# Kernel optimization log

Measured on AMD Instinct MI355X. Metric: run time of the kernel, lower is better.

The kernel has to match this reference:

```python
import jax, jax.numpy as jnp
import numpy as np

BIT = 128
Y_P = 0.5
RIGHT = BIT / 8.0
LEFT = RIGHT / 2.0
UB = BIT / 2.0
ALPHA = 0.1
PCT_NUM, PCT_DEN = 9, 10  # percent = 9/10
C_COEF = (1.0 / RIGHT) * np.log(Y_P / (99.0 * (1.0 - Y_P)))  # slope c (constant since y_p fixed)
A_COEF = -1.0 / (LEFT * C_COEF) * np.log(99.0 * Y_P / (1.0 - Y_P))  # hard-branch factor a
# with y_p=0.5: d = -c*BP, g = -a*c*BP, so f_easy = c*(x-BP), f_hard = a*c*(x-BP)


def setup_inputs() -> dict:
    key = jax.random.key(0)
    k1, k2 = jax.random.split(key)
    N, C = 6144, 200
    u = jax.random.normal(k1, (N, BIT), dtype=jnp.float32)
    labels = jax.random.randint(k2, (N,), 0, C)
    y = jax.nn.one_hot(labels, C, dtype=jnp.int32)
    ind = jnp.arange(N, dtype=jnp.int32)  # unused dataset indices
    return {"u": u, "y": y, "ind": ind}


def reference(u, y, ind):
    sg = jax.lax.stop_gradient
    N = u.shape[0]
    uh = jnp.tanh(u)
    s = (y @ y.T) > 0                      # [N,N] bool similarity (diagonal is True)
    inner = uh @ uh.T                      # [N,N]
    n_sim = s.sum(axis=1)                  # int per-row similar count
    n_dis = N - n_sim
    fn_sim = n_sim.astype(jnp.float32)
    fn_dis = n_dis.astype(jnp.float32)
    idx = jnp.arange(N)[None, :]

    meanS = jnp.clip(jnp.where(s, inner, 0.0).sum(1) / jnp.maximum(fn_sim, 1.0), 0.0, UB)
    meanDS = jnp.clip(jnp.where(s, 0.0, inner).sum(1) / jnp.maximum(fn_dis, 1.0), 0.0, UB)

    dis_sorted = jnp.sort(jnp.where(s, -jnp.inf, inner), axis=1)
    start_dis = (n_dis * PCT_NUM) // PCT_DEN          # int(len*0.9)
    tail_mask = idx >= (N - n_dis + start_dis)[:, None]
    tail_cnt = jnp.maximum((n_dis - start_dis).astype(jnp.float32), 1.0)
    dMax = jnp.clip(jnp.where(tail_mask, dis_sorted, 0.0).sum(1) / tail_cnt, 0.0, UB)

    sim_sorted = jnp.sort(jnp.where(s, inner, jnp.inf), axis=1)
    start_sim = (n_sim * PCT_NUM) // PCT_DEN
    head_mask = idx < (n_sim - start_sim)[:, None]
    head_cnt = jnp.maximum((n_sim - start_sim).astype(jnp.float32), 1.0)
    sMin = jnp.clip(jnp.where(head_mask, sim_sorted, 0.0).sum(1) / head_cnt, 0.0, UB)

    # .item() in the original detaches these -> stop_gradient
    meanS, meanDS, dMax, sMin = map(sg, (meanS, meanDS, dMax, sMin))
    BP = meanS - (UB - meanS) / UB * jnp.abs(meanS - dMax)      # [N]
    BPd = meanDS + meanDS / UB * jnp.abs(meanDS - sMin)         # [N]

    # similar-pair loss: f + log(1+exp(-f)) == softplus(f)
    dc = inner - BP[:, None]
    f_sim = jnp.where(inner > BP[:, None], C_COEF * dc, A_COEF * C_COEF * dc)
    mask_sim = s & (inner != BP[:, None])             # == BP excluded in torch indexing
    cnt_sim = jnp.maximum(mask_sim.sum(1).astype(jnp.float32), 1.0)
    row_pos = jnp.where(mask_sim, jax.nn.softplus(f_sim), 0.0).sum(1) / cnt_sim

    # dissimilar-pair loss: log(1+exp(-f)) == softplus(-f)
    dcd = inner - BPd[:, None]
    f_dis = jnp.where(inner < BPd[:, None], C_COEF * dcd, A_COEF * C_COEF * dcd)
    mask_dis = (~s) & (inner != BPd[:, None])
    cnt_dis = jnp.maximum(mask_dis.sum(1).astype(jnp.float32), 1.0)
    row_neg = jnp.where(mask_dis, jax.nn.softplus(-f_dis), 0.0).sum(1) / cnt_dis

    valid = (n_sim > 0) & (n_dis > 0)
    count = valid.sum().astype(jnp.float32)
    posL = jnp.where(count > 0, jnp.where(valid, row_pos, 0.0).sum() / jnp.maximum(count, 1.0), 0.0)
    navL = jnp.where(count > 0, jnp.where(valid, row_neg, 0.0).sum() / jnp.maximum(count, 1.0), 0.0)

    q_loss = ALPHA * jnp.mean((uh - jnp.sign(uh)) ** 2)
    return posL + navL + q_loss
```

## Files before the change

### kernel.cpp

```cpp
#include <hip/hip_runtime.h>
#include <cstdint>

#define NROW 6144
#define KDIM 128
#define NLAB 200
#define C_COEF (-0.28719499063341177f)
#define UBV 64.0f

typedef _Float16 f16x8 __attribute__((ext_vector_type(8)));
typedef _Float16 f16x2 __attribute__((ext_vector_type(2)));
typedef float f32x4 __attribute__((ext_vector_type(4)));
typedef __attribute__((address_space(1))) const void as1c_void;
typedef __attribute__((address_space(3))) void as3_void;

union U8 { f16x8 h; unsigned u[4]; f16x2 p[4]; };
union CV16 { _Float16 h; unsigned short us; };

__device__ __forceinline__ float softplus_f(float x){
  return fmaxf(x, 0.f) + __logf(1.f + __expf(-fabsf(x)));
}
__device__ __forceinline__ float waveRedF(float v){
#pragma unroll
  for (int o = 32; o; o >>= 1) v += __shfl_down(v, o, 64);
  return v;
}
__device__ __forceinline__ float bfRedF(float v){
#pragma unroll
  for (int o = 32; o; o >>= 1) v += __shfl_xor(v, o, 64);
  return v;
}
__device__ __forceinline__ int bfRedI(int v){
#pragma unroll
  for (int o = 32; o; o >>= 1) v += __shfl_xor(v, o, 64);
  return v;
}
__device__ __forceinline__ int bfMaxI(int v){
#pragma unroll
  for (int o = 32; o; o >>= 1){ int x = __shfl_xor(v, o, 64); v = v > x ? v : x; }
  return v;
}
__device__ __forceinline__ float bfMaxF(float v){
#pragma unroll
  for (int o = 32; o; o >>= 1) v = fmaxf(v, __shfl_xor(v, o, 64));
  return v;
}
__device__ __forceinline__ float val_of_key(unsigned key){
  unsigned bits = (key & 0x8000u) ? (key ^ 0x8000u) : (key ^ 0xFFFFu);
  CV16 cv; cv.us = (unsigned short)bits;
  return (float)cv.h;
}

__global__ __launch_bounds__(256) void k_labtanh(const int* __restrict__ y,
    unsigned char* __restrict__ lab, int* __restrict__ cnt, int* __restrict__ simIdx,
    const float* __restrict__ u, _Float16* __restrict__ uhswz, float* __restrict__ accf){
  const int bid = blockIdx.x;
  const int tid = threadIdx.x;
  const int NLB = NROW / 4;
  if (bid < NLB){
    const int lane = tid & 63;
    const int row = bid * 4 + (tid >> 6);
    if (lane < NLAB / 4){
      const int4 v = ((const int4*)(y + (size_t)row * NLAB))[lane];
      int t = -1;
      if (v.x != 0) t = 4 * lane;
      if (v.y != 0) t = 4 * lane + 1;
      if (v.z != 0) t = 4 * lane + 2;
      if (v.w != 0) t = 4 * lane + 3;
      if (t >= 0){
        lab[row] = (unsigned char)t;
        int p = atomicAdd(&cnt[t], 1);
        if (p < 512) simIdx[t * 512 + p] = row;
      }
    }
    return;
  }
  const int gid = (bid - NLB) * 256 + tid;
  const int row = gid >> 4;
  const int h = gid & 15;
  const int g = h ^ (row & 7);
  const float* sp = u + (size_t)row * KDIM + g * 8;
  float q = 0.f;
  f16x8 o;
#pragma unroll
  for (int t = 0; t < 8; t++){
    float x = sp[t];
    float e2 = __expf(2.f * x);
    float th = 1.f - 2.f * __builtin_amdgcn_rcpf(e2 + 1.f);
    float sg = (th > 0.f) ? 1.f : ((th < 0.f) ? -1.f : 0.f);
    float d = th - sg;
    q += d * d;
    o[t] = (_Float16)th;
  }
  *(f16x8*)(uhswz + (size_t)row * KDIM + h * 8) = o;
  q = waveRedF(q);
  __shared__ float qb[4];
  if ((tid & 63) == 0) qb[tid >> 6] = q;
  __syncthreads();
  if (tid == 0) atomicAdd(&accf[0], qb[0] + qb[1] + qb[2] + qb[3]);
}

__global__ __launch_bounds__(256) void k_mm(const _Float16* __restrict__ A,
    _Float16* __restrict__ out, int row0, int sym){
  const int bj = blockIdx.x, bi = blockIdx.y;
  if (sym && bi > bj) return;
  __shared__ __align__(16) _Float16 SH[2 * 128 * KDIM];
  _Float16* As = SH;
  _Float16* Bs = SH + 128 * KDIM;
  const int tid = threadIdx.x;
  const int wav = tid >> 6, lane = tid & 63;

  const char* Ag = (const char*)(A + (size_t)(row0 + bi * 128) * KDIM);
  const char* Bg = (const char*)(A + (size_t)(bj * 128) * KDIM);
  char* Asb = (char*)As;
  char* Bsb = (char*)Bs;
#pragma unroll
  for (int t = 0; t < 8; t++){
    const int ub = wav * 8192 + t * 1024;
    __builtin_amdgcn_global_load_lds((as1c_void*)(Ag + ub + lane * 16),
                                     (as3_void*)(Asb + ub), 16, 0, 0);
    __builtin_amdgcn_global_load_lds((as1c_void*)(Bg + ub + lane * 16),
                                     (as3_void*)(Bsb + ub), 16, 0, 0);
  }
  __syncthreads();

  const int quad = lane >> 4, l16 = lane & 15;
  const int wm = (wav >> 1) * 64, wn = (wav & 1) * 64;
  f32x4 acc[4][4];
#pragma unroll
  for (int im = 0; im < 4; im++)
#pragma unroll
    for (int in = 0; in < 4; in++)
      acc[im][in] = (f32x4){0.f, 0.f, 0.f, 0.f};

#pragma unroll
  for (int kb = 0; kb < 4; kb++){
    f16x8 af[4], bf[4];
#pragma unroll
    for (int i = 0; i < 4; i++){
      const int m = wm + i * 16 + l16;
      const int gidx = kb * 4 + quad;
      af[i] = *(const f16x8*)(Asb + m * 256 + ((gidx ^ (m & 7)) << 4));
      const int n = wn + i * 16 + l16;
      bf[i] = *(const f16x8*)(Bsb + n * 256 + ((gidx ^ (n & 7)) << 4));
    }
#pragma unroll
    for (int im = 0; im < 4; im++)
#pragma unroll
      for (int in = 0; in < 4; in++)
        acc[im][in] = __builtin_amdgcn_mfma_f32_16x16x32_f16(af[im], bf[in], acc[im][in], 0, 0, 0);
  }
  __syncthreads();

  _Float16* Cs = SH;
#pragma unroll
  for (int im = 0; im < 4; im++)
#pragma unroll
    for (int in = 0; in < 4; in++)
#pragma unroll
      for (int r = 0; r < 4; r++){
        const int rl = wm + im * 16 + quad * 4 + r;
        const int cl = wn + in * 16 + l16;
        Cs[rl * 132 + cl] = (_Float16)acc[im][in][r];
      }
  __syncthreads();

  _Float16* obase = out + (size_t)(bi * 128) * NROW + (size_t)bj * 128;
  const int s = tid & 15;
#pragma unroll
  for (int i = 0; i < 8; i++){
    const int r = (tid >> 4) + i * 16;
    f16x8 vv = *(const f16x8*)(Cs + r * 132 + s * 8);
    *(f16x8*)(obase + (size_t)r * NROW + s * 8) = vv;
  }

  if (sym && bi != bj){
    __syncthreads();
#pragma unroll
    for (int im = 0; im < 4; im++)
#pragma unroll
      for (int in = 0; in < 4; in++)
#pragma unroll
        for (int r = 0; r < 4; r++){
          const int rl = wm + im * 16 + quad * 4 + r;
          const int cl = wn + in * 16 + l16;
          Cs[cl * 132 + rl] = (_Float16)acc[im][in][r];
        }
    __syncthreads();
    _Float16* obase2 = out + (size_t)(bj * 128) * NROW + (size_t)bi * 128;
#pragma unroll
    for (int i = 0; i < 8; i++){
      const int r = (tid >> 4) + i * 16;
      f16x8 vv = *(const f16x8*)(Cs + r * 132 + s * 8);
      *(f16x8*)(obase2 + (size_t)r * NROW + s * 8) = vv;
    }
  }
}

__global__ __launch_bounds__(256) void k_stats(const _Float16* __restrict__ buf,
    const unsigned char* __restrict__ lab, const int* __restrict__ cnt,
    const int* __restrict__ simIdx, float* __restrict__ rowRes, int row0){
  __shared__ int   histS[4][1028];
  __shared__ float simvS[4][512];
  const int tid = threadIdx.x;
  const int lane = tid & 63;
  const int wav = tid >> 6;
  const int lrow = blockIdx.x * 4 + wav;
  const int row = row0 + lrow;
  const int myl = lab[row];
  const int n_sim = cnt[myl];
  const int n_dis = NROW - n_sim;
  if (n_dis == 0 || n_sim == 0) return;
  const int k1 = n_dis - (n_dis * 9) / 10;
  const int k2 = n_sim - (n_sim * 9) / 10;
  const int ns = (n_sim < 512) ? n_sim : 512;

  int*   hist = histS[wav];
  int*   myh  = hist + (lane >> 4) * 257;
  float* simv = simvS[wav];
#pragma unroll
  for (int r = 0; r < 4; r++) *(int4*)&hist[(lane + 64 * r) * 4] = make_int4(0, 0, 0, 0);
  if (lane == 0) *(int4*)&hist[1024] = make_int4(0, 0, 0, 0);

  const f16x8* src = (const f16x8*)(buf + (size_t)lrow * NROW);
  const _Float16* srcs = buf + (size_t)lrow * NROW;

  float sumAll = 0.f;
  const f16x2 ones = (f16x2){(_Float16)1.f, (_Float16)1.f};
#pragma unroll 2
  for (int it = 0; it < 12; ++it){
    U8 x; x.h = src[it * 64 + lane];
#pragma unroll
    for (int k = 0; k < 4; k++){
      unsigned wv = x.u[k];
      unsigned m = (wv >> 15) & 0x00010001u;
      unsigned key2 = wv ^ 0x80008000u ^ (m * 0x7FFFu);
      atomicAdd(&myh[(key2 >> 8) & 0xFFu], 1);
      atomicAdd(&myh[key2 >> 24], 1);
#if __has_builtin(__builtin_amdgcn_fdot2)
      sumAll = __builtin_amdgcn_fdot2(x.p[k], ones, sumAll, false);
#else
      sumAll += (float)x.h[2 * k] + (float)x.h[2 * k + 1];
#endif
    }
  }

  float sumS = 0.f;
  for (int t = lane; t < ns; t += 64){
    int idx = simIdx[myl * 512 + t];
    CV16 cv; cv.h = srcs[idx];
    unsigned bits = (unsigned)cv.us;
    unsigned key = bits ^ 0x8000u ^ ((bits >> 15) * 0x7FFFu);
    float v = (float)cv.h;
    simv[t] = v; sumS += v;
    atomicAdd(&myh[key >> 8], -1);
  }
  sumAll = bfRedF(sumAll);
  sumS = bfRedF(sumS);
  const float sumD = sumAll - sumS;

  int cArr[4];
#pragma unroll
  for (int d = 0; d < 4; d++){
    const int b = 4 * lane + d;
    cArr[d] = hist[b] + hist[257 + b] + hist[514 + b] + hist[771 + b];
  }
  int part = cArr[0] + cArr[1] + cArr[2] + cArr[3];
  int suf = part;
#pragma unroll
  for (int o = 1; o < 64; o <<= 1){
    int x = __shfl_down(suf, o, 64);
    if (lane + o < 64) suf += x;
  }
  int cum = suf - part;
  int encB = -1, krF = 0;
#pragma unroll
  for (int d = 3; d >= 0; --d){
    int cd = cArr[d];
    if (k1 > cum && k1 <= cum + cd){ encB = 4 * lane + d; krF = k1 - cum; }
    cum += cd;
  }
  const int hbStar = bfMaxI(encB);
  const int kr1 = bfMaxI(krF);

#pragma unroll
  for (int r = 0; r < 4; r++) *(int4*)&hist[(lane + 64 * r) * 4] = make_int4(0, 0, 0, 0);
  if (lane == 0) *(int4*)&hist[1024] = make_int4(0, 0, 0, 0);

  float sAb = 0.f;
#pragma unroll 2
  for (int it = 0; it < 12; ++it){
    U8 x; x.h = src[it * 64 + lane];
#pragma unroll
    for (int k = 0; k < 4; k++){
      unsigned wv = x.u[k];
      unsigned m = (wv >> 15) & 0x00010001u;
      unsigned key2 = wv ^ 0x80008000u ^ (m * 0x7FFFu);
      int hbLo = (key2 >> 8) & 0xFF;
      int hbHi = key2 >> 24;
      if (hbLo > hbStar) sAb += (float)x.h[2 * k];
      else if (hbLo == hbStar) atomicAdd(&myh[key2 & 0xFFu], 1);
      if (hbHi > hbStar) sAb += (float)x.h[2 * k + 1];
      else if (hbHi == hbStar) atomicAdd(&myh[(key2 >> 16) & 0xFFu], 1);
    }
  }
  for (int t = lane; t < ns; t += 64){
    float v = simv[t];
    CV16 cv; cv.h = (_Float16)v;
    unsigned bits = (unsigned)cv.us;
    unsigned key = bits ^ 0x8000u ^ ((bits >> 15) * 0x7FFFu);
    int hb = (int)(key >> 8);
    if (hb > hbStar) sAb -= v;
    else if (hb == hbStar) atomicAdd(&myh[key & 0xFFu], -1);
  }
  sAb = bfRedF(sAb);

  int c2[4];
#pragma unroll
  for (int d = 0; d < 4; d++){
    const int b = 4 * lane + d;
    c2[d] = hist[b] + hist[257 + b] + hist[514 + b] + hist[771 + b];
  }
  part = c2[0] + c2[1] + c2[2] + c2[3];
  suf = part;
#pragma unroll
  for (int o = 1; o < 64; o <<= 1){
    int x = __shfl_down(suf, o, 64);
    if (lane + o < 64) suf += x;
  }
  cum = suf - part;
  int encL = -1, g2F = 0;
#pragma unroll
  for (int d = 3; d >= 0; --d){
    int cd = c2[d];
    if (kr1 > cum && kr1 <= cum + cd){ encL = 4 * lane + d; g2F = cum; }
    cum += cd;
  }
  const int lbStar = bfMaxI(encL);
  const int gt2 = bfMaxI(g2F);
  float sumIn = 0.f;
#pragma unroll
  for (int d = 0; d < 4; d++){
    int lb = 4 * lane + d;
    if (lb > lbStar) sumIn += (float)c2[d] * val_of_key((unsigned)((hbStar << 8) | lb));
  }
  sumIn = bfRedF(sumIn);
  const float piv = val_of_key((unsigned)((hbStar << 8) | lbStar));
  const float dSum = sAb + sumIn + (float)(kr1 - gt2) * piv;

  float fpiv2 = -3e38f; int flt = 0;
  for (int t = lane; t < ns; t += 64){
    float vt = simv[t];
    int lt = 0, eq = 0;
    for (int j = 0; j < ns; j++){
      float vj = simv[j];
      lt += (vj < vt); eq += (vj == vt);
    }
    if (lt < k2 && k2 <= lt + eq){ fpiv2 = vt; flt = lt; }
  }
  const float piv2 = bfMaxF(fpiv2);
  const int ltS = bfMaxI(flt);
  float slt = 0.f;
  for (int t = lane; t < ns; t += 64){
    float v = simv[t];
    if (v < piv2) slt += v;
  }
  slt = bfRedF(slt);
  const float sSum = slt + (float)(k2 - ltS) * piv2;

  const float meanS  = fminf(fmaxf(sumS / fmaxf((float)n_sim, 1.f), 0.f), UBV);
  const float meanDS = fminf(fmaxf(sumD / fmaxf((float)n_dis, 1.f), 0.f), UBV);
  const float dMax   = fminf(fmaxf(dSum / fmaxf((float)k1, 1.f), 0.f), UBV);
  const float sMin   = fminf(fmaxf(sSum / fmaxf((float)k2, 1.f), 0.f), UBV);
  const float BP  = meanS - (UBV - meanS) / UBV * fabsf(meanS - dMax);
  const float BPd = meanDS + meanDS / UBV * fabsf(meanDS - sMin);

  float an = 0.f; int ties = 0;
#pragma unroll 2
  for (int it = 0; it < 12; ++it){
    f16x8 h8 = src[it * 64 + lane];
#pragma unroll
    for (int e = 0; e < 8; e++){
      float v = (float)h8[e];
      float dcd = v - BPd;
      float f = ((dcd < 0.f) ? C_COEF : 2.f * C_COEF) * dcd;
      an += softplus_f(-f);
      ties += (dcd == 0.f);
    }
  }
  float spSim = 0.f; int tiesSim = 0;
  float ap = 0.f, cp = 0.f;
  for (int t = lane; t < ns; t += 64){
    float v = simv[t];
    float dcd = v - BPd;
    if (dcd == 0.f) tiesSim++;
    else {
      float f = ((dcd < 0.f) ? C_COEF : 2.f * C_COEF) * dcd;
      spSim += softplus_f(-f);
    }
    if (v != BP){
      float dc = v - BP;
      float f = (v > BP) ? C_COEF * dc : (2.f * C_COEF) * dc;
      ap += softplus_f(f); cp += 1.f;
    }
  }
  an = bfRedF(an); spSim = bfRedF(spSim);
  const int tiesT = bfRedI(ties);
  const int tiesSimT = bfRedI(tiesSim);
  ap = bfRedF(ap); cp = bfRedF(cp);
  if (lane == 0){
    const float L = __logf(1.f + __expf(-0.f));
    float anF = an - (float)tiesT * L - spSim;
    float cnF = (float)(n_dis - (tiesT - tiesSimT));
    float4 r;
    r.x = ap / fmaxf(cp, 1.f);
    r.y = anF / fmaxf(cnF, 1.f);
    r.z = 1.f;
    r.w = 0.f;
    *(float4*)(rowRes + 4 * (size_t)row) = r;
  }
}

__global__ __launch_bounds__(256) void k_final(const float* __restrict__ accf,
    const float* __restrict__ rowRes, float* __restrict__ out){
  const int tid = threadIdx.x;
  float p = 0.f, n = 0.f, c = 0.f;
  for (int i = tid; i < NROW; i += 256){
    float4 r = *(const float4*)(rowRes + 4 * (size_t)i);
    p += r.x; n += r.y; c += r.z;
  }
  p = bfRedF(p); n = bfRedF(n); c = bfRedF(c);
  __shared__ float sb[12];
  const int wav = tid >> 6;
  if ((tid & 63) == 0){ sb[wav] = p; sb[4 + wav] = n; sb[8 + wav] = c; }
  __syncthreads();
  if (tid == 0){
    p = sb[0] + sb[1] + sb[2] + sb[3];
    n = sb[4] + sb[5] + sb[6] + sb[7];
    c = sb[8] + sb[9] + sb[10] + sb[11];
    float posL = 0.f, navL = 0.f;
    if (c > 0.f){ posL = p / c; navL = n / c; }
    out[0] = posL + navL + 0.1f * (accf[0] / (float)(NROW * KDIM));
  }
}

extern "C" void kernel_launch(void* const* d_in, const int* in_sizes, int n_in,
                              void* d_out, int out_size, void* d_ws, size_t ws_size,
                              hipStream_t stream){
  const float* u = (const float*)d_in[0];
  const int* y = (const int*)d_in[1];
  char* ws = (char*)d_ws;
  float* accf = (float*)ws;
  int* cnt = (int*)(ws + 64);
  float* rowRes = (float*)(ws + 4096);
  unsigned char* lab = (unsigned char*)(ws + 102400);
  int* simIdx = (int*)(ws + 108544);
  _Float16* uhswz = (_Float16*)(ws + 518144);
  const size_t ibufOff = 518144 + (size_t)NROW * KDIM * 2;
  _Float16* ibuf = (_Float16*)(ws + ibufOff);

  hipMemsetAsync(d_ws, 0, 102400, stream);
  k_labtanh<<<NROW / 4 + (NROW * 16) / 256, 256, 0, stream>>>(y, lab, cnt, simIdx,
                                                              u, uhswz, accf);

  size_t avail = (ws_size > ibufOff) ? ws_size - ibufOff : 0;
  long maxRows = (long)(avail / ((size_t)NROW * 2));
  maxRows = (maxRows / 128) * 128;
  if (maxRows > NROW) maxRows = NROW;
  if (maxRows < 128) maxRows = 128;

  for (int r0 = 0; r0 < NROW; r0 += (int)maxRows){
    int rows = NROW - r0;
    if (rows > maxRows) rows = (int)maxRows;
    const int sym = (rows == NROW) ? 1 : 0;
    k_mm<<<dim3(48, rows / 128), 256, 0, stream>>>(uhswz, ibuf, r0, sym);
    k_stats<<<rows / 4, 256, 0, stream>>>(ibuf, lab, cnt, simIdx, rowRes, r0);
  }
  k_final<<<1, 256, 0, stream>>>(accf, rowRes, (float*)d_out);
}
```

Baseline: 168.6 us.

## Launch only upper-triangle GEMM tiles with 512-thread blocks and shared diagonal loads

The symmetric Gram matrix kernel now launches exactly the 1176 upper-triangular 128x128 tiles, mapped from a linear block index, instead of a full 48x48 grid in which most lower blocks exit immediately. Blocks grow to 512 threads (8 waves each owning a 64x32 sub-tile), which halves per-wave accumulator registers and raises the number of waves per tile. Diagonal tiles load the operand tile once and reuse it for both A and B. The linear-to-triangular index mapping uses a serial loop of up to 48 iterations per block, and per-wave MFMA work per LDS fragment is lower.

```diff
diff --git a/kernel.cpp b/kernel.cpp
--- a/kernel.cpp
+++ b/kernel.cpp
@@ -99,63 +99,73 @@
   if (tid == 0) atomicAdd(&accf[0], qb[0] + qb[1] + qb[2] + qb[3]);
 }
 
-__global__ __launch_bounds__(256) void k_mm(const _Float16* __restrict__ A,
+__global__ __launch_bounds__(512) void k_mm(const _Float16* __restrict__ A,
     _Float16* __restrict__ out, int row0, int sym){
-  const int bj = blockIdx.x, bi = blockIdx.y;
-  if (sym && bi > bj) return;
+  int bi, bj;
+  if (sym){
+    int t = blockIdx.x;
+    int b = 0, off = 0;
+    while (t >= off + (48 - b)){ off += 48 - b; b++; }
+    bi = b; bj = b + (t - off);
+  } else {
+    bi = blockIdx.y; bj = blockIdx.x;
+  }
   __shared__ __align__(16) _Float16 SH[2 * 128 * KDIM];
-  _Float16* As = SH;
-  _Float16* Bs = SH + 128 * KDIM;
   const int tid = threadIdx.x;
   const int wav = tid >> 6, lane = tid & 63;
+  const bool diag = sym && (bi == bj);
 
   const char* Ag = (const char*)(A + (size_t)(row0 + bi * 128) * KDIM);
   const char* Bg = (const char*)(A + (size_t)(bj * 128) * KDIM);
-  char* Asb = (char*)As;
-  char* Bsb = (char*)Bs;
-#pragma unroll
-  for (int t = 0; t < 8; t++){
-    const int ub = wav * 8192 + t * 1024;
+  char* Asb = (char*)SH;
+  char* Bsb = diag ? Asb : (char*)(SH + 128 * KDIM);
+#pragma unroll
+  for (int t = 0; t < 4; t++){
+    const int ub = wav * 4096 + t * 1024;
     __builtin_amdgcn_global_load_lds((as1c_void*)(Ag + ub + lane * 16),
                                      (as3_void*)(Asb + ub), 16, 0, 0);
-    __builtin_amdgcn_global_load_lds((as1c_void*)(Bg + ub + lane * 16),
-                                     (as3_void*)(Bsb + ub), 16, 0, 0);
+    if (!diag)
+      __builtin_amdgcn_global_load_lds((as1c_void*)(Bg + ub + lane * 16),
+                                       (as3_void*)(Bsb + ub), 16, 0, 0);
   }
   __syncthreads();
 
   const int quad = lane >> 4, l16 = lane & 15;
-  const int wm = (wav >> 1) * 64, wn = (wav & 1) * 64;
-  f32x4 acc[4][4];
+  const int wm = (wav >> 2) * 64, wn = (wav & 3) * 32;
+  f32x4 acc[4][2];
 #pragma unroll
   for (int im = 0; im < 4; im++)
 #pragma unroll
-    for (int in = 0; in < 4; in++)
+    for (int in = 0; in < 2; in++)
       acc[im][in] = (f32x4){0.f, 0.f, 0.f, 0.f};
 
 #pragma unroll
   for (int kb = 0; kb < 4; kb++){
-    f16x8 af[4], bf[4];
+    f16x8 af[4], bf[2];
+    const int gidx = kb * 4 + quad;
 #pragma unroll
     for (int i = 0; i < 4; i++){
       const int m = wm + i * 16 + l16;
-      const int gidx = kb * 4 + quad;
       af[i] = *(const f16x8*)(Asb + m * 256 + ((gidx ^ (m & 7)) << 4));
-      const int n = wn + i * 16 + l16;
-      bf[i] = *(const f16x8*)(Bsb + n * 256 + ((gidx ^ (n & 7)) << 4));
+    }
+#pragma unroll
+    for (int j = 0; j < 2; j++){
+      const int n = wn + j * 16 + l16;
+      bf[j] = *(const f16x8*)(Bsb + n * 256 + ((gidx ^ (n & 7)) << 4));
     }
 #pragma unroll
     for (int im = 0; im < 4; im++)
 #pragma unroll
-      for (int in = 0; in < 4; in++)
+      for (int in = 0; in < 2; in++)
         acc[im][in] = __builtin_amdgcn_mfma_f32_16x16x32_f16(af[im], bf[in], acc[im][in], 0, 0, 0);
   }
   __syncthreads();
 
-  _Float16* Cs = SH;
+  _Float16* Cs = (_Float16*)SH;
 #pragma unroll
   for (int im = 0; im < 4; im++)
 #pragma unroll
-    for (int in = 0; in < 4; in++)
+    for (int in = 0; in < 2; in++)
 #pragma unroll
       for (int r = 0; r < 4; r++){
         const int rl = wm + im * 16 + quad * 4 + r;
@@ -166,9 +176,10 @@
 
   _Float16* obase = out + (size_t)(bi * 128) * NROW + (size_t)bj * 128;
   const int s = tid & 15;
-#pragma unroll
-  for (int i = 0; i < 8; i++){
-    const int r = (tid >> 4) + i * 16;
+  const int rb = tid >> 4;
+#pragma unroll
+  for (int i = 0; i < 4; i++){
+    const int r = rb + i * 32;
     f16x8 vv = *(const f16x8*)(Cs + r * 132 + s * 8);
     *(f16x8*)(obase + (size_t)r * NROW + s * 8) = vv;
   }
@@ -178,7 +189,7 @@
 #pragma unroll
     for (int im = 0; im < 4; im++)
 #pragma unroll
-      for (int in = 0; in < 4; in++)
+      for (int in = 0; in < 2; in++)
 #pragma unroll
         for (int r = 0; r < 4; r++){
           const int rl = wm + im * 16 + quad * 4 + r;
@@ -188,8 +199,8 @@
     __syncthreads();
     _Float16* obase2 = out + (size_t)(bj * 128) * NROW + (size_t)bi * 128;
 #pragma unroll
-    for (int i = 0; i < 8; i++){
-      const int r = (tid >> 4) + i * 16;
+    for (int i = 0; i < 4; i++){
+      const int r = rb + i * 32;
       f16x8 vv = *(const f16x8*)(Cs + r * 132 + s * 8);
       *(f16x8*)(obase2 + (size_t)r * NROW + s * 8) = vv;
     }
@@ -471,8 +482,11 @@
   for (int r0 = 0; r0 < NROW; r0 += (int)maxRows){
     int rows = NROW - r0;
     if (rows > maxRows) rows = (int)maxRows;
-    const int sym = (rows == NROW) ? 1 : 0;
-    k_mm<<<dim3(48, rows / 128), 256, 0, stream>>>(uhswz, ibuf, r0, sym);
+    if (rows == NROW){
+      k_mm<<<dim3(48 * 49 / 2), 512, 0, stream>>>(uhswz, ibuf, r0, 1);
+    } else {
+      k_mm<<<dim3(48, rows / 128), 512, 0, stream>>>(uhswz, ibuf, r0, 0);
+    }
     k_stats<<<rows / 4, 256, 0, stream>>>(ibuf, lab, cnt, simIdx, rowRes, r0);
   }
   k_final<<<1, 256, 0, stream>>>(accf, rowRes, (float*)d_out);
```

Result: faster. 165.1 us (-2.0%).
